# Kernel tuning notes

Measured on AMD Instinct MI355X. Metric: run time of the kernel, lower is better.

## Reference

```python
import jax, jax.numpy as jnp
import numpy as np
import math

D_MODEL = 1024
H = 16
D_K = D_MODEL // H
D_FF = 4096
NEG = -1e9


def layer_norm(x, alpha, bias):
    # Faithful to source: mean over last dim, UNBIASED std (torch.std default),
    # eps defined in source but never used in forward.
    mean = jnp.mean(x, axis=-1, keepdims=True)
    std = jnp.std(x, axis=-1, ddof=1, keepdims=True)
    return (x - mean) / std * alpha + bias


def mha(x, mask, w_q, w_k, w_v, w_o):
    B, S, D = x.shape
    q = (x @ w_q.T).reshape(B, S, H, D_K)
    k = (x @ w_k.T).reshape(B, S, H, D_K)
    v = (x @ w_v.T).reshape(B, S, H, D_K)
    scores = jnp.einsum('bqhd,bkhd->bhqk', q, k) / math.sqrt(D_K)
    scores = jnp.where(mask, NEG, scores)
    attn = jax.nn.softmax(scores, axis=-1)
    out = jnp.einsum('bhqk,bkhd->bqhd', attn, v).reshape(B, S, D)
    return out @ w_o.T


def setup_inputs() -> dict:
    key = jax.random.key(0)
    ks = jax.random.split(key, 16)
    B, S = 4, 2048
    s = 0.02
    return {
        'x': jax.random.normal(ks[0], (B, S, D_MODEL), jnp.float32),
        'w_q': jax.random.normal(ks[1], (D_MODEL, D_MODEL), jnp.float32) * s,
        'w_k': jax.random.normal(ks[2], (D_MODEL, D_MODEL), jnp.float32) * s,
        'w_v': jax.random.normal(ks[3], (D_MODEL, D_MODEL), jnp.float32) * s,
        'w_o': jax.random.normal(ks[4], (D_MODEL, D_MODEL), jnp.float32) * s,
        'l1_w': jax.random.normal(ks[5], (D_FF, D_MODEL), jnp.float32) * s,
        'l1_b': jnp.zeros((D_FF,), jnp.float32),
        'l2_w': jax.random.normal(ks[6], (D_MODEL, D_FF), jnp.float32) * s,
        'l2_b': jnp.zeros((D_MODEL,), jnp.float32),
        'norm1_a': jnp.ones((D_MODEL,), jnp.float32),
        'norm1_b': jnp.zeros((D_MODEL,), jnp.float32),
        'norm2_a': jnp.ones((D_MODEL,), jnp.float32),
        'norm2_b': jnp.zeros((D_MODEL,), jnp.float32),
        'normf_a': jnp.ones((D_MODEL,), jnp.float32),
        'normf_b': jnp.zeros((D_MODEL,), jnp.float32),
        'mask': jax.random.randint(ks[7], (B, 1, 1, S), 0, 2) == 1,
    }


def reference(x, w_q, w_k, w_v, w_o, l1_w, l1_b, l2_w, l2_b,
              norm1_a, norm1_b, norm2_a, norm2_b, normf_a, normf_b, mask):
    # residual 1: pre-norm self-attention (dropout is identity at eval)
    x = x + mha(layer_norm(x, norm1_a, norm1_b), mask, w_q, w_k, w_v, w_o)
    # residual 2: pre-norm FFN
    h = layer_norm(x, norm2_a, norm2_b)
    ff = jax.nn.relu(h @ l1_w.T + l1_b) @ l2_w.T + l2_b
    x = x + ff
    return layer_norm(x, normf_a, normf_b)
```

## Files before the change

kernel.cpp:

```cpp
#include <hip/hip_runtime.h>
#include <hip/hip_bf16.h>


typedef __bf16 bf16x8 __attribute__((ext_vector_type(8)));
typedef float f32x4 __attribute__((ext_vector_type(4)));
typedef unsigned short u16x8 __attribute__((ext_vector_type(8)));
using bf16 = __hip_bfloat16;

__device__ __forceinline__ f32x4 mfma16(bf16x8 a, bf16x8 b, f32x4 c) {
  return __builtin_amdgcn_mfma_f32_16x16x32_bf16(a, b, c, 0, 0, 0);
}

__device__ __forceinline__ int swz(int row, int blk) {
  return row * 64 + ((blk ^ (row & 7)) << 3);
}

__device__ __forceinline__ void stage_tile64(unsigned short* lds,
                                             const bf16* g, int ld, int rows) {
  const int lane = threadIdx.x & 63, wid = threadIdx.x >> 6;
  const int r8 = lane >> 3, blk = lane & 7;
  const bf16* gl = g + (size_t)r8 * ld + ((blk ^ r8) << 3);
  const int passes = rows >> 3;
  for (int p = wid; p < passes; p += 4) {
    __builtin_amdgcn_global_load_lds(
        (const __attribute__((address_space(1))) void*)(gl + (size_t)(p * 8) * ld),
        (__attribute__((address_space(3))) void*)(lds + p * 512),
        16, 0, 0);
  }
}

__device__ __forceinline__ void stage_half512(unsigned short* lds,
                                              const bf16* g, int ld) {
  const int lane = threadIdx.x & 63, w8 = threadIdx.x >> 6;
  const int r8 = lane >> 3, blk = lane & 7;
  const bf16* gl = g + (size_t)r8 * ld + ((blk ^ r8) << 3);
  __builtin_amdgcn_global_load_lds(
      (const __attribute__((address_space(1))) void*)(gl + (size_t)(w8 * 8) * ld),
      (__attribute__((address_space(3))) void*)(lds + w8 * 512), 16, 0, 0);
  __builtin_amdgcn_global_load_lds(
      (const __attribute__((address_space(1))) void*)(gl + (size_t)((w8 + 8) * 8) * ld),
      (__attribute__((address_space(3))) void*)(lds + (w8 + 8) * 512), 16, 0, 0);
}

__device__ __forceinline__ short bfb(float x) {
  return (short)__hip_bfloat16_raw(__float2bfloat16(x)).x;
}

__global__ __launch_bounds__(256) void cvt_k(const float* __restrict__ s,
                                             bf16* __restrict__ d, int n) {
  const int i = (blockIdx.x * 256 + threadIdx.x) * 4;
  if (i + 3 < n) {
    const float4 v = *reinterpret_cast<const float4*>(s + i);
    ushort4 o;
    o.x = (unsigned short)bfb(v.x);
    o.y = (unsigned short)bfb(v.y);
    o.z = (unsigned short)bfb(v.z);
    o.w = (unsigned short)bfb(v.w);
    *reinterpret_cast<ushort4*>(d + i) = o;
  }
}

template <bool OUT_F32>
__global__ __launch_bounds__(256) void layernorm_k(const float* __restrict__ in,
                                                   const float* __restrict__ gamma,
                                                   const float* __restrict__ beta,
                                                   void* __restrict__ out) {
  __shared__ float red[8];
  const int row = blockIdx.x, t = threadIdx.x;
  const float4 vv = reinterpret_cast<const float4*>(in + (size_t)row * 1024)[t];
  const float x0 = vv.x, x1 = vv.y, x2 = vv.z, x3 = vv.w;
  float s = x0 + x1 + x2 + x3;
#pragma unroll
  for (int off = 32; off; off >>= 1) s += __shfl_down(s, off);
  if ((t & 63) == 0) red[t >> 6] = s;
  __syncthreads();
  const float mean = (red[0] + red[1] + red[2] + red[3]) * (1.0f / 1024.0f);
  const float d0 = x0 - mean, d1 = x1 - mean, d2 = x2 - mean, d3 = x3 - mean;
  float sq = d0 * d0 + d1 * d1 + d2 * d2 + d3 * d3;
#pragma unroll
  for (int off = 32; off; off >>= 1) sq += __shfl_down(sq, off);
  if ((t & 63) == 0) red[4 + (t >> 6)] = sq;
  __syncthreads();
  const float var =
      fmaxf((red[4] + red[5] + red[6] + red[7]) * (1.0f / 1023.0f), 1e-20f);
  const float rstd = rsqrtf(var);
  const float4 ga = reinterpret_cast<const float4*>(gamma)[t];
  const float4 be = reinterpret_cast<const float4*>(beta)[t];
  const float y0 = d0 * rstd * ga.x + be.x;
  const float y1 = d1 * rstd * ga.y + be.y;
  const float y2 = d2 * rstd * ga.z + be.z;
  const float y3 = d3 * rstd * ga.w + be.w;
  if (OUT_F32) {
    reinterpret_cast<float4*>((float*)out + (size_t)row * 1024)[t] =
        make_float4(y0, y1, y2, y3);
  } else {
    ushort4 o;
    o.x = (unsigned short)bfb(y0);
    o.y = (unsigned short)bfb(y1);
    o.z = (unsigned short)bfb(y2);
    o.w = (unsigned short)bfb(y3);
    reinterpret_cast<ushort4*>((bf16*)out + (size_t)row * 1024)[t] = o;
  }
}

template <bool HAS_BIAS, bool RELU, bool HAS_RES, bool OUT_F32>
__global__ __launch_bounds__(256) void gemm_bt(const bf16* __restrict__ A,
                                               const bf16* __restrict__ W,
                                               const float* __restrict__ bias,
                                               const float* __restrict__ resid,
                                               void* __restrict__ out,
                                               int M, int N, int K,
                                               int lda, int ldw) {
  __shared__ __align__(16) unsigned short As[128 * 64];
  __shared__ __align__(16) unsigned short Bs[128 * 64];
  const int lane = threadIdx.x & 63, wid = threadIdx.x >> 6;
  const int n16 = lane & 15, quad = lane >> 4;
  const int wm = (wid >> 1) * 64, wn = (wid & 1) * 64;
  const int tm = blockIdx.x * 128, tn = blockIdx.y * 128;
  f32x4 acc[4][4] = {};
  for (int k0 = 0; k0 < K; k0 += 64) {
    stage_tile64(As, A + (size_t)tm * lda + k0, lda, 128);
    stage_tile64(Bs, W + (size_t)tn * ldw + k0, ldw, 128);
    __syncthreads();
#pragma unroll
    for (int kk = 0; kk < 64; kk += 32) {
      bf16x8 af[4], bw[4];
#pragma unroll
      for (int i = 0; i < 4; ++i)
        af[i] = *reinterpret_cast<const bf16x8*>(
            &As[swz(wm + i * 16 + n16, (kk >> 3) + quad)]);
#pragma unroll
      for (int j = 0; j < 4; ++j)
        bw[j] = *reinterpret_cast<const bf16x8*>(
            &Bs[swz(wn + j * 16 + n16, (kk >> 3) + quad)]);
#pragma unroll
      for (int i = 0; i < 4; ++i)
#pragma unroll
        for (int j = 0; j < 4; ++j) acc[i][j] = mfma16(af[i], bw[j], acc[i][j]);
    }
    __syncthreads();
  }
#pragma unroll
  for (int i = 0; i < 4; ++i) {
#pragma unroll
    for (int j = 0; j < 4; ++j) {
      const int n = tn + wn + j * 16 + n16;
      const float bv = HAS_BIAS ? bias[n] : 0.0f;
#pragma unroll
      for (int r = 0; r < 4; ++r) {
        const int m = tm + wm + i * 16 + quad * 4 + r;
        float vv = acc[i][j][r] + bv;
        if (RELU) vv = fmaxf(vv, 0.0f);
        if (HAS_RES) vv += resid[(size_t)m * N + n];
        if (OUT_F32)
          ((float*)out)[(size_t)m * N + n] = vv;
        else
          ((bf16*)out)[(size_t)m * N + n] = __float2bfloat16(vv);
      }
    }
  }
}

template <bool QKV, bool HAS_BIAS, bool RELU>
__global__ __launch_bounds__(512, 2) void gemm256_k(
    const bf16* __restrict__ A0, const bf16* __restrict__ cln,
    const bf16* __restrict__ W, const float* __restrict__ bias,
    const int* __restrict__ cnt, bf16* __restrict__ out,
    bf16* __restrict__ kvout, int M, int N, int K, int lda, int ldw) {
  __shared__ __align__(16) unsigned short Lds[65536];
  const int tm = blockIdx.x * 256;
  const int tn = blockIdx.y * 256;
  const bf16* A = A0;
  bool isQ = true;
  if (QKV) {
    isQ = (blockIdx.y < 4);
    if (!isQ) {
      const int npad = (cnt[tm >> 11] + 127) & ~127;
      if ((tm & 2047) >= npad) return;
      A = cln;
    }
  }
  const int lane = threadIdx.x & 63, w8 = threadIdx.x >> 6;
  const int n16 = lane & 15, quad = lane >> 4;
  const int wm = (w8 >> 2) << 7;
  const int wn = (w8 & 3) << 6;
  const int NT = K >> 6;
  const unsigned short* LAb = Lds + ((wm >> 7) * 8192);
  const unsigned short* LBb = Lds + 16384 + ((wn >> 7) * 8192);
  const int browB = wn & 127;
  f32x4 acc[8][4] = {};
#pragma unroll
  for (int pt = 0; pt < 2; ++pt) {
    unsigned short* base = Lds + pt * 32768;
    const bf16* Ag = A + (size_t)tm * lda + pt * 64;
    const bf16* Wg = W + (size_t)tn * ldw + pt * 64;
    stage_half512(base, Ag, lda);
    stage_half512(base + 8192, Ag + (size_t)128 * lda, lda);
    stage_half512(base + 16384, Wg, ldw);
    stage_half512(base + 24576, Wg + (size_t)128 * ldw, ldw);
  }
  for (int t = 0; t < NT; ++t) {
    const int bofs = (t & 1) * 32768;
    if (t + 1 < NT)
      asm volatile("s_waitcnt vmcnt(8)" ::: "memory");
    else
      asm volatile("s_waitcnt vmcnt(0)" ::: "memory");
    __builtin_amdgcn_sched_barrier(0);
    __builtin_amdgcn_s_barrier();
    const unsigned short* LA = LAb + bofs;
    const unsigned short* LB = LBb + bofs;
    bf16x8 bfr[4][2];
#pragma unroll
    for (int j = 0; j < 4; ++j) {
      const int br = browB + j * 16 + n16;
      bfr[j][0] = *reinterpret_cast<const bf16x8*>(&LB[swz(br, quad)]);
      bfr[j][1] = *reinterpret_cast<const bf16x8*>(&LB[swz(br, 4 + quad)]);
    }
#pragma unroll
    for (int ph = 0; ph < 4; ++ph) {
      bf16x8 af0[2], af1[2];
#pragma unroll
      for (int ii = 0; ii < 2; ++ii) {
        const int ar = (ph * 2 + ii) * 16 + n16;
        af0[ii] = *reinterpret_cast<const bf16x8*>(&LA[swz(ar, quad)]);
        af1[ii] = *reinterpret_cast<const bf16x8*>(&LA[swz(ar, 4 + quad)]);
      }
      __builtin_amdgcn_s_setprio(1);
#pragma unroll
      for (int ii = 0; ii < 2; ++ii)
#pragma unroll
        for (int j = 0; j < 4; ++j) {
          f32x4 c = acc[ph * 2 + ii][j];
          c = mfma16(af0[ii], bfr[j][0], c);
          c = mfma16(af1[ii], bfr[j][1], c);
          acc[ph * 2 + ii][j] = c;
        }
      __builtin_amdgcn_s_setprio(0);
      __builtin_amdgcn_s_barrier();
    }
    if (t + 2 < NT) {
      unsigned short* base = Lds + bofs;
      const bf16* Ag = A + (size_t)tm * lda + (t + 2) * 64;
      const bf16* Wg = W + (size_t)tn * ldw + (t + 2) * 64;
      stage_half512(base, Ag, lda);
      stage_half512(base + 8192, Ag + (size_t)128 * lda, lda);
      stage_half512(base + 16384, Wg, ldw);
      stage_half512(base + 24576, Wg + (size_t)128 * ldw, ldw);
    }
  }
  bf16* op;
  int ldo, nc0;
  if (QKV && !isQ) {
    op = kvout; ldo = 2048; nc0 = tn - 1024;
  } else if (QKV) {
    op = out; ldo = 1024; nc0 = tn;
  } else {
    op = out; ldo = N; nc0 = tn;
  }
#pragma unroll
  for (int i = 0; i < 8; ++i) {
#pragma unroll
    for (int j = 0; j < 4; ++j) {
      const int n = nc0 + wn + j * 16 + n16;
      const float bv = HAS_BIAS ? bias[n] : 0.0f;
#pragma unroll
      for (int r = 0; r < 4; ++r) {
        const int m = tm + wm + i * 16 + quad * 4 + r;
        float vv = acc[i][j][r] + bv;
        if (RELU) vv = fmaxf(vv, 0.0f);
        op[(size_t)m * ldo + n] = __float2bfloat16(vv);
      }
    }
  }
}

__global__ __launch_bounds__(256) void prep_mask_k(const int* __restrict__ m,
                                                   float* __restrict__ mf,
                                                   int n) {
  __shared__ int s;
  if (threadIdx.x == 0) s = 0;
  __syncthreads();
  unsigned int acc = 0;
  for (int i = threadIdx.x; i < 512; i += 256)
    acc |= ((const unsigned int*)m)[i] & 0xFFFFFF00u;
  if (acc) atomicOr(&s, 1);
  __syncthreads();
  const bool bytes = (s != 0);
  const int i = blockIdx.x * 256 + threadIdx.x;
  if (i < n) {
    const int v = bytes ? (int)((const unsigned char*)m)[i] : m[i];
    mf[i] = v ? -1.4427e9f : 0.0f;
  }
}

__global__ __launch_bounds__(256) void scan_k(const float* __restrict__ maskf,
                                              float* __restrict__ cmask,
                                              int* __restrict__ idx,
                                              int* __restrict__ cnt) {
  __shared__ int wsum[4];
  const int b = blockIdx.x, t = threadIdx.x, lane = t & 63, w = t >> 6;
  const float* mrow = maskf + b * 2048;
  int keep[8], local = 0;
#pragma unroll
  for (int e = 0; e < 8; ++e) {
    keep[e] = (mrow[t * 8 + e] == 0.0f) ? 1 : 0;
    local += keep[e];
  }
  int inc = local;
#pragma unroll
  for (int off = 1; off < 64; off <<= 1) {
    int v = __shfl_up(inc, off);
    if (lane >= off) inc += v;
  }
  if (lane == 63) wsum[w] = inc;
  __syncthreads();
  int base = 0;
#pragma unroll
  for (int i = 0; i < 4; ++i)
    if (i < w) base += wsum[i];
  int p = base + inc - local;
#pragma unroll
  for (int e = 0; e < 8; ++e)
    if (keep[e]) idx[b * 2048 + p++] = t * 8 + e;
  const int total = wsum[0] + wsum[1] + wsum[2] + wsum[3];
  if (t == 0) cnt[b] = total;
  for (int i = t; i < 2048; i += 256)
    cmask[b * 2048 + i] = (i < total) ? 0.0f : -1.4427e9f;
}

__global__ __launch_bounds__(128) void gatherA_k(const bf16* __restrict__ ln1,
                                                 const int* __restrict__ idx,
                                                 const int* __restrict__ cnt,
                                                 bf16* __restrict__ cln) {
  const int b = blockIdx.x >> 11, j = blockIdx.x & 2047;
  const int n = cnt[b];
  const int npad = (n + 127) & ~127;
  if (j >= npad) return;
  u16x8* dst = reinterpret_cast<u16x8*>(cln + ((size_t)(b * 2048 + j)) * 1024);
  if (j < n) {
    const int s = idx[b * 2048 + j];
    const u16x8* src =
        reinterpret_cast<const u16x8*>(ln1 + ((size_t)(b * 2048 + s)) * 1024);
    dst[threadIdx.x] = src[threadIdx.x];
  } else {
    u16x8 z = {};
    dst[threadIdx.x] = z;
  }
}

__global__ __launch_bounds__(256) void attn_k(const bf16* __restrict__ q,
                                              const bf16* __restrict__ kv,
                                              const float* __restrict__ cmask,
                                              const int* __restrict__ cnt,
                                              bf16* __restrict__ out, int BHN) {
  __shared__ __align__(16) unsigned short Ks[2][64 * 64];
  __shared__ __align__(16) unsigned short Vs[2][64 * 72];
  const int lane = threadIdx.x & 63, wid = threadIdx.x >> 6;
  const int n16 = lane & 15, quad = lane >> 4;
  const int bid = blockIdx.x;
  const int bh = bid % BHN, qb = bid / BHN;
  const int b = bh >> 4, h = bh & 15;
  const bf16* qp0 = q + (size_t)b * 2048 * 1024 + h * 64;
  const bf16* kp0 = kv + (size_t)b * 2048 * 2048 + h * 64;
  const bf16* vp0 = kp0 + 1024;
  const float* mfb = cmask + b * 2048;
  const int cntb = cnt[b];
  const int nk = ((cntb + 63) >> 6) << 6;
  const int qrow0 = qb * 128 + wid * 32;

  bf16x8 qf[2][2];
#pragma unroll
  for (int g = 0; g < 2; ++g) {
    const bf16* qp = qp0 + (size_t)(qrow0 + g * 16 + n16) * 1024 + quad * 8;
    qf[g][0] = *reinterpret_cast<const bf16x8*>(qp);
    qf[g][1] = *reinterpret_cast<const bf16x8*>(qp + 32);
  }
  bf16x8 ones;
#pragma unroll
  for (int e = 0; e < 8; ++e) ones[e] = (__bf16)1.0f;
  f32x4 oacc[2][4] = {};
  f32x4 lacc[2] = {};
  const int prow = ((n16 >> 2) << 3) + (n16 & 3);
  const int vkey = lane, vdc = wid * 16;

  stage_tile64(Ks[0], kp0, 2048, 64);
  {
    const bf16* vp = vp0 + (size_t)vkey * 2048 + vdc;
    const u16x8 a = *reinterpret_cast<const u16x8*>(vp);
    const u16x8 bq = *reinterpret_cast<const u16x8*>(vp + 8);
#pragma unroll
    for (int e = 0; e < 8; ++e) {
      Vs[0][(vdc + e) * 72 + vkey] = a[e];
      Vs[0][(vdc + 8 + e) * 72 + vkey] = bq[e];
    }
  }
  int cur = 0;
  for (int kt = 0; kt < nk; kt += 64) {
    __syncthreads();
    const bool hasNext = (kt + 64 < nk);
    const bool fullTile = (kt + 64 <= cntb);
    u16x8 na = {}, nb = {};
    if (hasNext) {
      stage_tile64(Ks[cur ^ 1], kp0 + (size_t)(kt + 64) * 2048, 2048, 64);
      const bf16* vp = vp0 + (size_t)(kt + 64 + vkey) * 2048 + vdc;
      na = *reinterpret_cast<const u16x8*>(vp);
      nb = *reinterpret_cast<const u16x8*>(vp + 8);
    }
    const unsigned short* Kc = Ks[cur];
    const unsigned short* Vc = Vs[cur];
#pragma unroll
    for (int sub = 0; sub < 2; ++sub) {
      const int kb = sub * 32;
      bf16x8 aflo[2], afhi[2];
#pragma unroll
      for (int st = 0; st < 2; ++st) {
        const int row = kb + prow + st * 4;
        aflo[st] = *reinterpret_cast<const bf16x8*>(&Kc[swz(row, quad)]);
        afhi[st] = *reinterpret_cast<const bf16x8*>(&Kc[swz(row, 4 + quad)]);
      }
      __builtin_amdgcn_s_setprio(1);
      f32x4 z[2][2];
#pragma unroll
      for (int g = 0; g < 2; ++g)
#pragma unroll
        for (int st = 0; st < 2; ++st) {
          f32x4 zz = {};
          zz = mfma16(aflo[st], qf[g][0], zz);
          zz = mfma16(afhi[st], qf[g][1], zz);
          z[g][st] = zz;
        }
      __builtin_amdgcn_s_setprio(0);
      float4 m0 = make_float4(0.f, 0.f, 0.f, 0.f);
      float4 m1 = make_float4(0.f, 0.f, 0.f, 0.f);
      if (!fullTile) {
        m0 = *reinterpret_cast<const float4*>(mfb + kt + kb + quad * 8);
        m1 = *reinterpret_cast<const float4*>(mfb + kt + kb + quad * 8 + 4);
      }
      bf16x8 vf[4];
#pragma unroll
      for (int j = 0; j < 4; ++j)
        vf[j] = *reinterpret_cast<const bf16x8*>(
            &Vc[(j * 16 + n16) * 72 + kb + quad * 8]);
#pragma unroll
      for (int g = 0; g < 2; ++g) {
        bf16x8 pf;
#pragma unroll
        for (int r = 0; r < 4; ++r) {
          const float e0 = __builtin_amdgcn_exp2f(
              fmaf(z[g][0][r], 0.18033688f, ((const float*)&m0)[r]));
          const float e1 = __builtin_amdgcn_exp2f(
              fmaf(z[g][1][r], 0.18033688f, ((const float*)&m1)[r]));
          pf[r] = (__bf16)e0;
          pf[4 + r] = (__bf16)e1;
        }
        __builtin_amdgcn_s_setprio(1);
#pragma unroll
        for (int j = 0; j < 4; ++j) oacc[g][j] = mfma16(pf, vf[j], oacc[g][j]);
        lacc[g] = mfma16(pf, ones, lacc[g]);
        __builtin_amdgcn_s_setprio(0);
      }
    }
    if (hasNext) {
      unsigned short* Vn = Vs[cur ^ 1];
#pragma unroll
      for (int e = 0; e < 8; ++e) {
        Vn[(vdc + e) * 72 + vkey] = na[e];
        Vn[(vdc + 8 + e) * 72 + vkey] = nb[e];
      }
    }
    cur ^= 1;
  }
#pragma unroll
  for (int g = 0; g < 2; ++g) {
#pragma unroll
    for (int r = 0; r < 4; ++r) {
      const float lr = 1.0f / fmaxf(lacc[g][r], 1e-20f);
      bf16* op =
          out + (size_t)(b * 2048 + qrow0 + g * 16 + quad * 4 + r) * 1024 +
          h * 64;
#pragma unroll
      for (int j = 0; j < 4; ++j)
        op[j * 16 + n16] = __float2bfloat16(oacc[g][j][r] * lr);
    }
  }
}

extern "C" void kernel_launch(void* const* d_in, const int* in_sizes, int n_in,
                              void* d_out, int out_size, void* d_ws,
                              size_t ws_size, hipStream_t stream) {
  const float* x    = (const float*)d_in[0];
  const float* w_q  = (const float*)d_in[1];
  const float* w_k  = (const float*)d_in[2];
  const float* w_v  = (const float*)d_in[3];
  const float* w_o  = (const float*)d_in[4];
  const float* l1_w = (const float*)d_in[5];
  const float* l1_b = (const float*)d_in[6];
  const float* l2_w = (const float*)d_in[7];
  const float* l2_b = (const float*)d_in[8];
  const float* n1a  = (const float*)d_in[9];
  const float* n1b  = (const float*)d_in[10];
  const float* n2a  = (const float*)d_in[11];
  const float* n2b  = (const float*)d_in[12];
  const float* nfa  = (const float*)d_in[13];
  const float* nfb  = (const float*)d_in[14];
  const int* mask   = (const int*)d_in[15];

  const int D = 1024, FF = 4096;
  const int M = in_sizes[0] / D;
  const int B = M / 2048;

  const size_t MB = 1024ull * 1024ull;
  if (ws_size < 121 * MB) return;
  char* w = (char*)d_ws;
  bf16* WQKV = (bf16*)(w + 0 * MB);
  bf16* WO   = (bf16*)(w + 6 * MB);
  bf16* L1W  = (bf16*)(w + 8 * MB);
  bf16* L2W  = (bf16*)(w + 16 * MB);
  bf16* LN1  = (bf16*)(w + 24 * MB);
  bf16* Qbuf = (bf16*)(w + 40 * MB);
  bf16* ATT  = LN1;
  bf16* HLN  = (bf16*)(w + 40 * MB);
  bf16* CLN  = (bf16*)(w + 56 * MB);
  bf16* FF1  = (bf16*)(w + 56 * MB);
  bf16* KV   = (bf16*)(w + 88 * MB);
  float* X1  = (float*)(w + 88 * MB);
  float* MASKF = (float*)(w + 120 * MB);
  float* CMASK = (float*)(w + 120 * MB + 256 * 1024);
  int*   IDX   = (int*)(w + 120 * MB + 512 * 1024);
  int*   CNT   = (int*)(w + 120 * MB + 768 * 1024);

  const dim3 blk(256);
  cvt_k<<<dim3(D * D / 1024), blk, 0, stream>>>(w_q, WQKV, D * D);
  cvt_k<<<dim3(D * D / 1024), blk, 0, stream>>>(w_k, WQKV + D * D, D * D);
  cvt_k<<<dim3(D * D / 1024), blk, 0, stream>>>(w_v, WQKV + 2 * D * D, D * D);
  cvt_k<<<dim3(D * D / 1024), blk, 0, stream>>>(w_o, WO, D * D);
  cvt_k<<<dim3(FF * D / 1024), blk, 0, stream>>>(l1_w, L1W, FF * D);
  cvt_k<<<dim3(FF * D / 1024), blk, 0, stream>>>(l2_w, L2W, FF * D);
  prep_mask_k<<<dim3((M + 255) / 256), blk, 0, stream>>>(mask, MASKF, M);
  scan_k<<<dim3(B), blk, 0, stream>>>(MASKF, CMASK, IDX, CNT);

  layernorm_k<false><<<M, blk, 0, stream>>>(x, n1a, n1b, LN1);
  gatherA_k<<<dim3(B * 2048), dim3(128), 0, stream>>>(LN1, IDX, CNT, CLN);
  gemm256_k<true, false, false><<<dim3(M / 256, 12), dim3(512), 0, stream>>>(
      LN1, CLN, WQKV, nullptr, CNT, Qbuf, KV, M, 3072, 1024, 1024, 1024);
  const int BHN = B * 16;
  attn_k<<<dim3((M / 128) * 16), blk, 0, stream>>>(Qbuf, KV, CMASK, CNT, ATT,
                                                   BHN);
  gemm_bt<false, false, true, true><<<dim3(M / 128, D / 128), blk, 0, stream>>>(
      ATT, WO, nullptr, x, X1, M, D, D, D, D);
  layernorm_k<false><<<M, blk, 0, stream>>>(X1, n2a, n2b, HLN);
  for (int c = 0; c < 2; ++c) {
    gemm256_k<false, true, true><<<dim3(M / 256, 8), dim3(512), 0, stream>>>(
        HLN, nullptr, L1W + (size_t)c * 2048 * D, l1_b + c * 2048, nullptr,
        FF1, nullptr, M, 2048, 1024, 1024, 1024);
    if (c == 0)
      gemm_bt<true, false, true, true>
          <<<dim3(M / 128, D / 128), blk, 0, stream>>>(
              FF1, L2W + c * 2048, l2_b, X1, X1, M, D, 2048, 2048, FF);
    else
      gemm_bt<false, false, true, true>
          <<<dim3(M / 128, D / 128), blk, 0, stream>>>(
              FF1, L2W + c * 2048, nullptr, X1, X1, M, D, 2048, 2048, FF);
  }
  layernorm_k<true><<<M, blk, 0, stream>>>(X1, nfa, nfb, (float*)d_out);
}
```

Measured before the change: 516.6 us.

## Interleave per-region global-to-LDS staging with MFMA phases in 256-tile GEMM

Restructures the 256x256 GEMM main loop into an unrolled two-tile schedule. Each quarter-phase issues one region's global_load_lds for a future tile right after its LDS fragment reads, instead of staging all four regions in a burst after the compute. The goal is to spread memory traffic evenly across the MFMA work and hide load latency, with barriers and waitcnts placed per phase. It adds more barriers, and correctness depends on K/64 being even and on the vmcnt accounting being right.

New measurement: 504.9 us. 2.3% less time.

```diff
diff --git a/kernel.cpp b/kernel.cpp
--- a/kernel.cpp
+++ b/kernel.cpp
@@ -161,16 +161,53 @@
   }
 }
 
+#define PHASE(BUFSEL, Q, DO_B, STAGE_STMT, WAIT_STMT)                          \
+  {                                                                            \
+    const unsigned short* LA = Lds + (BUFSEL)*32768 + lasel * 8192;            \
+    if (DO_B) {                                                                \
+      const unsigned short* LB =                                               \
+          Lds + (BUFSEL)*32768 + 16384 + lbsel * 8192;                         \
+      _Pragma("unroll") for (int j = 0; j < 4; ++j) {                          \
+        const int br = bloc + j * 16 + n16;                                    \
+        bfr[j][0] = *reinterpret_cast<const bf16x8*>(&LB[swz(br, quad)]);      \
+        bfr[j][1] = *reinterpret_cast<const bf16x8*>(&LB[swz(br, 4 + quad)]);  \
+      }                                                                        \
+    }                                                                          \
+    bf16x8 a0[2], a1[2];                                                       \
+    _Pragma("unroll") for (int ii = 0; ii < 2; ++ii) {                         \
+      const int ar = ((Q)*2 + ii) * 16 + n16;                                  \
+      a0[ii] = *reinterpret_cast<const bf16x8*>(&LA[swz(ar, quad)]);           \
+      a1[ii] = *reinterpret_cast<const bf16x8*>(&LA[swz(ar, 4 + quad)]);       \
+    }                                                                          \
+    STAGE_STMT;                                                                \
+    WAIT_STMT;                                                                 \
+    __builtin_amdgcn_sched_barrier(0);                                         \
+    __builtin_amdgcn_s_barrier();                                              \
+    asm volatile("s_waitcnt lgkmcnt(0)" ::: "memory");                         \
+    __builtin_amdgcn_sched_barrier(0);                                         \
+    __builtin_amdgcn_s_setprio(1);                                             \
+    _Pragma("unroll") for (int ii = 0; ii < 2; ++ii)                           \
+        _Pragma("unroll") for (int j = 0; j < 4; ++j) {                        \
+      f32x4 c = acc[(Q)*2 + ii][j];                                            \
+      c = mfma16(a0[ii], bfr[j][0], c);                                        \
+      c = mfma16(a1[ii], bfr[j][1], c);                                        \
+      acc[(Q)*2 + ii][j] = c;                                                  \
+    }                                                                          \
+    __builtin_amdgcn_s_setprio(0);                                             \
+    __builtin_amdgcn_sched_barrier(0);                                         \
+    __builtin_amdgcn_s_barrier();                                              \
+  }
+
 template <bool QKV, bool HAS_BIAS, bool RELU>
 __global__ __launch_bounds__(512, 2) void gemm256_k(
-    const bf16* __restrict__ A0, const bf16* __restrict__ cln,
+    const bf16* __restrict__ A0p, const bf16* __restrict__ cln,
     const bf16* __restrict__ W, const float* __restrict__ bias,
     const int* __restrict__ cnt, bf16* __restrict__ out,
     bf16* __restrict__ kvout, int M, int N, int K, int lda, int ldw) {
   __shared__ __align__(16) unsigned short Lds[65536];
   const int tm = blockIdx.x * 256;
   const int tn = blockIdx.y * 256;
-  const bf16* A = A0;
+  const bf16* A = A0p;
   bool isQ = true;
   if (QKV) {
     isQ = (blockIdx.y < 4);
@@ -184,69 +221,41 @@
   const int n16 = lane & 15, quad = lane >> 4;
   const int wm = (w8 >> 2) << 7;
   const int wn = (w8 & 3) << 6;
-  const int NT = K >> 6;
-  const unsigned short* LAb = Lds + ((wm >> 7) * 8192);
-  const unsigned short* LBb = Lds + 16384 + ((wn >> 7) * 8192);
-  const int browB = wn & 127;
+  const int lasel = wm >> 7, lbsel = wn >> 7, bloc = wn & 127;
+  const int NTT = K >> 6;
+  const bf16* Ag = A + (size_t)tm * lda;
+  const bf16* Wg = W + (size_t)tn * ldw;
   f32x4 acc[8][4] = {};
-#pragma unroll
-  for (int pt = 0; pt < 2; ++pt) {
-    unsigned short* base = Lds + pt * 32768;
-    const bf16* Ag = A + (size_t)tm * lda + pt * 64;
-    const bf16* Wg = W + (size_t)tn * ldw + pt * 64;
-    stage_half512(base, Ag, lda);
-    stage_half512(base + 8192, Ag + (size_t)128 * lda, lda);
-    stage_half512(base + 16384, Wg, ldw);
-    stage_half512(base + 24576, Wg + (size_t)128 * ldw, ldw);
-  }
-  for (int t = 0; t < NT; ++t) {
-    const int bofs = (t & 1) * 32768;
-    if (t + 1 < NT)
-      asm volatile("s_waitcnt vmcnt(8)" ::: "memory");
+
+  auto STAGE = [&](int bufsel, int region, int tile) {
+    unsigned short* dst = Lds + bufsel * 32768 + region * 8192;
+    if (region < 2)
+      stage_half512(dst, Ag + (size_t)(region * 128) * lda + tile * 64, lda);
     else
-      asm volatile("s_waitcnt vmcnt(0)" ::: "memory");
-    __builtin_amdgcn_sched_barrier(0);
-    __builtin_amdgcn_s_barrier();
-    const unsigned short* LA = LAb + bofs;
-    const unsigned short* LB = LBb + bofs;
+      stage_half512(dst, Wg + (size_t)((region - 2) * 128) * ldw + tile * 64,
+                    ldw);
+  };
+
+  STAGE(0, 0, 0); STAGE(0, 1, 0); STAGE(0, 2, 0); STAGE(0, 3, 0);
+  STAGE(1, 2, 1); STAGE(1, 3, 1);
+  asm volatile("s_waitcnt vmcnt(4)" ::: "memory");
+  __builtin_amdgcn_sched_barrier(0);
+  __builtin_amdgcn_s_barrier();
+
+  for (int i = 0; i < NTT; i += 2) {
+    const bool hasNext = (i + 2 < NTT);
     bf16x8 bfr[4][2];
-#pragma unroll
-    for (int j = 0; j < 4; ++j) {
-      const int br = browB + j * 16 + n16;
-      bfr[j][0] = *reinterpret_cast<const bf16x8*>(&LB[swz(br, quad)]);
-      bfr[j][1] = *reinterpret_cast<const bf16x8*>(&LB[swz(br, 4 + quad)]);
-    }
-#pragma unroll
-    for (int ph = 0; ph < 4; ++ph) {
-      bf16x8 af0[2], af1[2];
-#pragma unroll
-      for (int ii = 0; ii < 2; ++ii) {
-        const int ar = (ph * 2 + ii) * 16 + n16;
-        af0[ii] = *reinterpret_cast<const bf16x8*>(&LA[swz(ar, quad)]);
-        af1[ii] = *reinterpret_cast<const bf16x8*>(&LA[swz(ar, 4 + quad)]);
-      }
-      __builtin_amdgcn_s_setprio(1);
-#pragma unroll
-      for (int ii = 0; ii < 2; ++ii)
-#pragma unroll
-        for (int j = 0; j < 4; ++j) {
-          f32x4 c = acc[ph * 2 + ii][j];
-          c = mfma16(af0[ii], bfr[j][0], c);
-          c = mfma16(af1[ii], bfr[j][1], c);
-          acc[ph * 2 + ii][j] = c;
-        }
-      __builtin_amdgcn_s_setprio(0);
-      __builtin_amdgcn_s_barrier();
-    }
-    if (t + 2 < NT) {
-      unsigned short* base = Lds + bofs;
-      const bf16* Ag = A + (size_t)tm * lda + (t + 2) * 64;
-      const bf16* Wg = W + (size_t)tn * ldw + (t + 2) * 64;
-      stage_half512(base, Ag, lda);
-      stage_half512(base + 8192, Ag + (size_t)128 * lda, lda);
-      stage_half512(base + 16384, Wg, ldw);
-      stage_half512(base + 24576, Wg + (size_t)128 * ldw, ldw);
-    }
+    PHASE(0, 0, true, STAGE(1, 0, i + 1), );
+    PHASE(0, 1, false, STAGE(1, 1, i + 1), );
+    PHASE(0, 2, false, if (hasNext) STAGE(0, 2, i + 2), );
+    PHASE(0, 3, false, if (hasNext) STAGE(0, 3, i + 2),
+          if (hasNext) { asm volatile("s_waitcnt vmcnt(4)" ::: "memory"); }
+          else { asm volatile("s_waitcnt vmcnt(0)" ::: "memory"); });
+    PHASE(1, 0, true, if (hasNext) STAGE(0, 0, i + 2), );
+    PHASE(1, 1, false, if (hasNext) STAGE(0, 1, i + 2), );
+    PHASE(1, 2, false, if (hasNext) STAGE(1, 2, i + 3), );
+    PHASE(1, 3, false, if (hasNext) STAGE(1, 3, i + 3),
+          if (hasNext) { asm volatile("s_waitcnt vmcnt(4)" ::: "memory"); });
   }
   bf16* op;
   int ldo, nc0;
```
